# Kernel optimization log

Measured on AMD Instinct MI355X. Metric: run time of the kernel, lower is better.

Reference implementation:

```python
import jax, jax.numpy as jnp
import numpy as np

D_MODEL = 1024
NHEAD = 16
HEAD_DIM = D_MODEL // NHEAD
B, L = 4, 8192
LN_EPS = 1e-5


def setup_inputs() -> dict:
    key = jax.random.key(0)
    ks = jax.random.split(key, 8)
    s = 1.0 / np.sqrt(D_MODEL)
    return {
        "x": jax.random.normal(ks[0], (B, L, D_MODEL), dtype=jnp.float32),
        "decay": jax.random.uniform(ks[1], (NHEAD,), dtype=jnp.float32, minval=0.8, maxval=0.999),
        "Wq": jax.random.normal(ks[2], (D_MODEL, D_MODEL), dtype=jnp.float32) * s,
        "Wv": jax.random.normal(ks[3], (D_MODEL, D_MODEL), dtype=jnp.float32) * s,
        "Wg": jax.random.normal(ks[4], (D_MODEL, D_MODEL), dtype=jnp.float32) * s,
        "Wo": jax.random.normal(ks[5], (D_MODEL, D_MODEL), dtype=jnp.float32) * s,
        "ln_gamma": jnp.ones((D_MODEL,), dtype=jnp.float32),
        "ln_beta": jnp.zeros((D_MODEL,), dtype=jnp.float32),
    }


def _decay_scan(v, lam):
    # v: (B, L, H, Dh), lam: (H,). s_t = lam * s_{t-1} + v_t, parallel assoc scan over L.
    a = jnp.broadcast_to(lam[None, None, :, None], v.shape)

    def combine(c1, c2):
        a1, b1 = c1
        a2, b2 = c2
        return a1 * a2, b1 * a2 + b2

    _, state = jax.lax.associative_scan(combine, (a, v), axis=1)
    return state


def _layernorm(y, gamma, beta):
    mu = jnp.mean(y, axis=-1, keepdims=True)
    var = jnp.mean(jnp.square(y - mu), axis=-1, keepdims=True)
    return (y - mu) * jax.lax.rsqrt(var + LN_EPS) * gamma + beta


def reference(x, decay, Wq, Wv, Wg, Wo, ln_gamma, ln_beta):
    Bx, Lx, D = x.shape
    q = (x @ Wq.T).reshape(Bx, Lx, NHEAD, HEAD_DIM)
    v = (x @ Wv.T).reshape(Bx, Lx, NHEAD, HEAD_DIM)
    state = _decay_scan(v, decay)                      # (B, L, H, Dh)
    y = (q * state).reshape(Bx, Lx, D)
    y = _layernorm(y, ln_gamma, ln_beta)
    gate = jax.nn.silu(x @ Wg.T)
    y = y * gate
    return y @ Wo.T
```

## Files before the change

kernel.cpp:

```cpp
#include <hip/hip_runtime.h>
#include <cstdint>
#include <cstddef>

typedef unsigned short u16;
typedef __attribute__((ext_vector_type(4))) float f32x4;
typedef __attribute__((ext_vector_type(8))) short s16x8;
typedef __attribute__((ext_vector_type(4))) short s16x4;

#define D_M   1024
#define KDIM  1024
#define BB    4
#define LL    8192
#define MTOT  (BB*LL)
#define CHK   64
#define CHK_SH 6
#define NCH   (LL/CHK)
#define NT    (KDIM/64)
#define LN_EPS 1e-5f

static __device__ __forceinline__ float bf2f(u16 u){
  return __uint_as_float(((unsigned)u)<<16);
}
static __device__ __forceinline__ u16 f2bf(float f){
  unsigned u = __float_as_uint(f);
  u += 0x7fffu + ((u>>16)&1u);
  return (u16)(u>>16);
}

template<int IMM>
static __device__ __forceinline__ s16x8 dsr(uint32_t a){
  s16x8 d;
  asm volatile("ds_read_b128 %0, %1 offset:%c2" : "=v"(d) : "v"(a), "i"(IMM));
  return d;
}

__global__ void conv_f2b_k(const float* __restrict__ src, u16* __restrict__ dst, int n4){
  int i = blockIdx.x*blockDim.x + threadIdx.x;
  int stride = gridDim.x*blockDim.x;
  for (; i < n4; i += stride){
    f32x4 f = ((const f32x4*)src)[i];
    s16x4 o;
    o[0]=(short)f2bf(f[0]); o[1]=(short)f2bf(f[1]);
    o[2]=(short)f2bf(f[2]); o[3]=(short)f2bf(f[3]);
    ((s16x4*)dst)[i] = o;
  }
}

__global__ void conv_w4_k(const float* __restrict__ s0, const float* __restrict__ s1,
                          const float* __restrict__ s2, const float* __restrict__ s3,
                          u16* __restrict__ d0, u16* __restrict__ d1,
                          u16* __restrict__ d2, u16* __restrict__ d3){
  const float* s; u16* d;
  switch(blockIdx.y){
    case 0: s=s0; d=d0; break;
    case 1: s=s1; d=d1; break;
    case 2: s=s2; d=d2; break;
    default: s=s3; d=d3; break;
  }
  int i = blockIdx.x*blockDim.x + threadIdx.x;
  f32x4 f = ((const f32x4*)s)[i];
  s16x4 o;
  o[0]=(short)f2bf(f[0]); o[1]=(short)f2bf(f[1]);
  o[2]=(short)f2bf(f[2]); o[3]=(short)f2bf(f[3]);
  ((s16x4*)d)[i] = o;
}

template<int F32OUT>
__global__ __launch_bounds__(512,2) void gemm256(
    const u16* __restrict__ A,
    const u16* __restrict__ W0, const u16* __restrict__ W1, const u16* __restrict__ W2,
    void* __restrict__ O0, void* __restrict__ O1, void* __restrict__ O2)
{
  __shared__ __align__(16) u16 smem[65536];

  const int mode = blockIdx.z;
  const u16* W = (mode==0)? W0 : ((mode==1)? W1 : W2);
  void* Ov     = (mode==0)? O0 : ((mode==1)? O1 : O2);

  const int tid  = threadIdx.x;
  const int wave = tid>>6, lane = tid&63;
  const int bm = blockIdx.x*256, bn = blockIdx.y*256;

  const int rr = tid>>3;
  const int kk = (((tid&7) ^ (rr&7)))*8;
  const int ldw = wave*512;

  #define STAGE(GBASE, LOFF) do {                                                       \
    const u16* _g = (GBASE) + (size_t)rr*KDIM + kk;                                     \
    __builtin_amdgcn_global_load_lds(                                                   \
      (const __attribute__((address_space(1))) void*)(_g),                              \
      (__attribute__((address_space(3))) void*)(smem + (LOFF) + ldw), 16, 0, 0);        \
    __builtin_amdgcn_global_load_lds(                                                   \
      (const __attribute__((address_space(1))) void*)(_g + (size_t)64*KDIM),            \
      (__attribute__((address_space(3))) void*)(smem + (LOFF) + 4096 + ldw), 16, 0, 0); \
  } while(0)

  const uint32_t smem_base =
    (uint32_t)(uintptr_t)((__attribute__((address_space(3))) u16*)smem);
  const int lr = lane&15, lk = lane>>4;
  const int wm = wave>>2, wn = wave&3;
  const uint32_t vA0 = smem_base + (uint32_t)((((wm*64+lr)*64) + (( lk   )^(lr&7))*8)<<1);
  const uint32_t vA1 = smem_base + (uint32_t)((((wm*64+lr)*64) + ((4+lk  )^(lr&7))*8)<<1);
  const uint32_t vB0 = smem_base + 65536u + (uint32_t)((((wn*32+lr)*64) + (( lk )^(lr&7))*8)<<1);
  const uint32_t vB1 = smem_base + 65536u + (uint32_t)((((wn*32+lr)*64) + ((4+lk)^(lr&7))*8)<<1);

  const f32x4 fzero = {0.f,0.f,0.f,0.f};
  f32x4 acc[8][4];
  #pragma unroll
  for (int i=0;i<8;i++)
    #pragma unroll
    for (int j=0;j<4;j++)
      acc[i][j] = fzero;

  const u16* Abase = A + (size_t)bm*KDIM;
  const u16* Wbase = W + (size_t)bn*KDIM;

  STAGE(Abase,                    0);
  STAGE(Wbase,                    32768);
  STAGE(Wbase + (size_t)128*KDIM, 32768+8192);
  STAGE(Abase + (size_t)128*KDIM, 8192);
  STAGE(Abase + 64,                    16384);
  STAGE(Wbase + 64,                    49152);
  STAGE(Wbase + (size_t)128*KDIM + 64, 49152+8192);
  asm volatile("s_waitcnt vmcnt(6)" ::: "memory");
  __builtin_amdgcn_s_barrier();

  s16x8 afr[4][2], blo[2][2], bhi[2][2];

  #define LDA8(CUR,HI) \
    afr[0][0]=dsr<(CUR)*32768+(HI)*16384+0   >(vA0); afr[0][1]=dsr<(CUR)*32768+(HI)*16384+0   >(vA1); \
    afr[1][0]=dsr<(CUR)*32768+(HI)*16384+2048>(vA0); afr[1][1]=dsr<(CUR)*32768+(HI)*16384+2048>(vA1); \
    afr[2][0]=dsr<(CUR)*32768+(HI)*16384+4096>(vA0); afr[2][1]=dsr<(CUR)*32768+(HI)*16384+4096>(vA1); \
    afr[3][0]=dsr<(CUR)*32768+(HI)*16384+6144>(vA0); afr[3][1]=dsr<(CUR)*32768+(HI)*16384+6144>(vA1);

  #define LDB4(DST,CUR,HI) \
    DST[0][0]=dsr<(CUR)*32768+(HI)*16384+0   >(vB0); DST[0][1]=dsr<(CUR)*32768+(HI)*16384+0   >(vB1); \
    DST[1][0]=dsr<(CUR)*32768+(HI)*16384+2048>(vB0); DST[1][1]=dsr<(CUR)*32768+(HI)*16384+2048>(vB1);

  #define LGKM_FENCE() do { \
    asm volatile("s_waitcnt lgkmcnt(0)" ::: "memory"); \
    __builtin_amdgcn_sched_barrier(0); \
  } while(0)

  #define MM16(AI0, NI0, BFR) \
    _Pragma("unroll") \
    for (int mi=0; mi<4; ++mi) \
      _Pragma("unroll") \
      for (int ni=0; ni<2; ++ni) \
        _Pragma("unroll") \
        for (int kp=0; kp<2; ++kp) \
          acc[(AI0)+mi][(NI0)+ni] = __builtin_amdgcn_mfma_f32_16x16x32_bf16( \
            afr[mi][kp], BFR[ni][kp], acc[(AI0)+mi][(NI0)+ni], 0,0,0);

  #define TILE(KT, CUR) do {                                                       \
                                        \
    LDA8(CUR,0)                                                                    \
    LDB4(blo,CUR,0)                                                                \
    if ((KT)+1 < NT) STAGE(Abase + (size_t)128*KDIM + ((KT)+1)*64,                 \
                           ((CUR)^1)*16384 + 8192);                                \
    __builtin_amdgcn_s_barrier();                                                  \
    LGKM_FENCE();                                                                  \
    __builtin_amdgcn_s_setprio(1);                                                 \
    MM16(0,0,blo)                                                                  \
    __builtin_amdgcn_s_setprio(0);                                                 \
    __builtin_amdgcn_s_barrier();                                                  \
                                        \
    LDB4(bhi,CUR,1)                                                                \
    if ((KT)+2 < NT) STAGE(Abase + ((KT)+2)*64, (CUR)*16384);                      \
    __builtin_amdgcn_s_barrier();                                                  \
    LGKM_FENCE();                                                                  \
    __builtin_amdgcn_s_setprio(1);                                                 \
    MM16(0,2,bhi)                                                                  \
    __builtin_amdgcn_s_setprio(0);                                                 \
    __builtin_amdgcn_s_barrier();                                                  \
                                        \
    LDA8(CUR,1)                                                                    \
    if ((KT)+2 < NT) STAGE(Wbase + ((KT)+2)*64, 32768 + (CUR)*16384);              \
    __builtin_amdgcn_s_barrier();                                                  \
    LGKM_FENCE();                                                                  \
    __builtin_amdgcn_s_setprio(1);                                                 \
    MM16(4,2,bhi)                                                                  \
    __builtin_amdgcn_s_setprio(0);                                                 \
    __builtin_amdgcn_s_barrier();                                                  \
                         \
    if ((KT)+2 < NT) STAGE(Wbase + (size_t)128*KDIM + ((KT)+2)*64,                 \
                           32768 + (CUR)*16384 + 8192);                            \
    __builtin_amdgcn_s_barrier();                                                  \
    __builtin_amdgcn_s_setprio(1);                                                 \
    MM16(4,0,blo)                                                                  \
    __builtin_amdgcn_s_setprio(0);                                                 \
    if ((KT) < NT-2) { asm volatile("s_waitcnt vmcnt(6)" ::: "memory"); }          \
    else             { asm volatile("s_waitcnt vmcnt(0)" ::: "memory"); }          \
    __builtin_amdgcn_s_barrier();                                                  \
  } while(0)

  for (int kt=0; kt<NT; kt+=2){
    TILE(kt,   0);
    TILE(kt+1, 1);
  }
  #undef TILE
  #undef MM16
  #undef LGKM_FENCE
  #undef LDB4
  #undef LDA8
  #undef STAGE

  const int rq = (lane>>4)*4;
  const int cl = lane&15;
  if (F32OUT){
    float* O = (float*)Ov;
    #pragma unroll
    for (int mi=0; mi<8; ++mi){
      const int grow = bm + (mi>>2)*128 + wm*64 + (mi&3)*16 + rq;
      #pragma unroll
      for (int ni=0; ni<4; ++ni){
        const int gcol = bn + (ni>>1)*128 + wn*32 + (ni&1)*16 + cl;
        #pragma unroll
        for (int r=0;r<4;r++)
          O[(size_t)(grow + r)*D_M + gcol] = acc[mi][ni][r];
      }
    }
  } else {
    u16* O = (u16*)Ov;
    const bool do_silu = (mode==2);
    #pragma unroll
    for (int mi=0; mi<8; ++mi){
      const int grow = bm + (mi>>2)*128 + wm*64 + (mi&3)*16 + rq;
      #pragma unroll
      for (int ni=0; ni<4; ++ni){
        const int gcol = bn + (ni>>1)*128 + wn*32 + (ni&1)*16 + cl;
        #pragma unroll
        for (int r=0;r<4;r++){
          float vv = acc[mi][ni][r];
          if (do_silu) vv = vv / (1.f + __expf(-vv));
          O[(size_t)(grow + r)*D_M + gcol] = f2bf(vv);
        }
      }
    }
  }
}

__global__ __launch_bounds__(256) void scan1_k(u16* __restrict__ v, float* __restrict__ E,
                                               const float* __restrict__ decay){
  const int c = blockIdx.x, b = blockIdx.y;
  const int d0 = threadIdx.x*4;
  const float lam = decay[d0>>6];
  float s0=0.f,s1=0.f,s2=0.f,s3=0.f;
  u16* p = v + ((size_t)b*LL + (size_t)c*CHK)*D_M + d0;
  for (int i=0;i<CHK;i++){
    s16x4 x = *(const s16x4*)p;
    s0 = fmaf(s0, lam, bf2f((u16)x[0]));
    s1 = fmaf(s1, lam, bf2f((u16)x[1]));
    s2 = fmaf(s2, lam, bf2f((u16)x[2]));
    s3 = fmaf(s3, lam, bf2f((u16)x[3]));
    s16x4 o;
    o[0]=(short)f2bf(s0); o[1]=(short)f2bf(s1);
    o[2]=(short)f2bf(s2); o[3]=(short)f2bf(s3);
    *(s16x4*)p = o;
    p += D_M;
  }
  f32x4 e = {s0,s1,s2,s3};
  *(f32x4*)(E + ((size_t)(b*NCH + c))*D_M + d0) = e;
}

__global__ void scan2_k(const float* __restrict__ E, float* __restrict__ S,
                        const float* __restrict__ decay){
  const int idx = blockIdx.x*blockDim.x + threadIdx.x;
  if (idx >= BB*(D_M/4)) return;
  const int b  = idx / (D_M/4);
  const int d0 = (idx % (D_M/4))*4;
  const float lam  = decay[d0>>6];
  const float lamT = __expf((float)CHK * __logf(lam));
  f32x4 s = {0.f,0.f,0.f,0.f};
  for (int c=0;c<NCH;c++){
    const size_t o = ((size_t)(b*NCH + c))*D_M + d0;
    f32x4 e = *(const f32x4*)(E + o);
    s = s*lamT + e;
    *(f32x4*)(S + o) = s;
  }
}

__global__ __launch_bounds__(256) void fuse_ln_k(
  const u16* __restrict__ qb, const u16* __restrict__ locb, const u16* __restrict__ gateb,
  const float* __restrict__ S, const float* __restrict__ decay,
  const float* __restrict__ gamma, const float* __restrict__ beta,
  u16* __restrict__ yout)
{
  const int token = blockIdx.x;
  const int b  = token >> 13;
  const int t  = token & (LL-1);
  const int c  = t >> CHK_SH;
  const int ii = t & (CHK-1);
  const int tid = threadIdx.x;
  const int d0 = tid*4;
  const float lam = decay[d0>>6];
  const float pw  = __expf((float)(ii+1) * __logf(lam));
  f32x4 carry = {0.f,0.f,0.f,0.f};
  if (c > 0) carry = *(const f32x4*)(S + ((size_t)(b*NCH + (c-1)))*D_M + d0);
  const size_t base = (size_t)token*D_M + d0;
  s16x4 q4 = *(const s16x4*)(qb + base);
  s16x4 l4 = *(const s16x4*)(locb + base);
  float y[4];
  #pragma unroll
  for (int j=0;j<4;j++)
    y[j] = bf2f((u16)q4[j]) * (bf2f((u16)l4[j]) + pw*carry[j]);
  float sum = y[0]+y[1]+y[2]+y[3];
  float sq  = y[0]*y[0]+y[1]*y[1]+y[2]*y[2]+y[3]*y[3];
  #pragma unroll
  for (int off=32; off>0; off>>=1){
    sum += __shfl_down(sum, off);
    sq  += __shfl_down(sq , off);
  }
  __shared__ float red[10];
  const int wave = tid>>6, lane = tid&63;
  if (lane==0){ red[wave] = sum; red[4+wave] = sq; }
  __syncthreads();
  if (tid==0){
    float ts = red[0]+red[1]+red[2]+red[3];
    float tq = red[4]+red[5]+red[6]+red[7];
    float mu  = ts * (1.f/(float)D_M);
    float var = tq * (1.f/(float)D_M) - mu*mu;
    red[8] = mu;
    red[9] = rsqrtf(var + LN_EPS);
  }
  __syncthreads();
  const float mu = red[8], rstd = red[9];
  f32x4 gm = *(const f32x4*)(gamma + d0);
  f32x4 bt = *(const f32x4*)(beta  + d0);
  s16x4 g4 = *(const s16x4*)(gateb + base);
  s16x4 o;
  #pragma unroll
  for (int j=0;j<4;j++){
    float nn = (y[j] - mu)*rstd*gm[j] + bt[j];
    nn *= bf2f((u16)g4[j]);
    o[j] = (short)f2bf(nn);
  }
  *(s16x4*)(yout + base) = o;
}

extern "C" void kernel_launch(void* const* d_in, const int* in_sizes, int n_in,
                              void* d_out, int out_size, void* d_ws, size_t ws_size,
                              hipStream_t stream)
{
  const float* x     = (const float*)d_in[0];
  const float* decay = (const float*)d_in[1];
  const float* Wq    = (const float*)d_in[2];
  const float* Wv    = (const float*)d_in[3];
  const float* Wg    = (const float*)d_in[4];
  const float* Wo    = (const float*)d_in[5];
  const float* gamma = (const float*)d_in[6];
  const float* beta  = (const float*)d_in[7];
  float* out = (float*)d_out;

  char* ws = (char*)d_ws;
  size_t off = 0;
  const size_t XB = (size_t)MTOT*D_M*sizeof(u16);
  const size_t WB = (size_t)D_M*KDIM*sizeof(u16);
  const size_t EB = (size_t)BB*NCH*D_M*sizeof(float);
  u16* xb  = (u16*)(ws+off); off += XB;
  u16* Wqb = (u16*)(ws+off); off += WB;
  u16* Wvb = (u16*)(ws+off); off += WB;
  u16* Wgb = (u16*)(ws+off); off += WB;
  u16* Wob = (u16*)(ws+off); off += WB;
  u16* qb  = (u16*)(ws+off); off += XB;
  u16* vb  = (u16*)(ws+off); off += XB;
  u16* gb  = (u16*)(ws+off); off += XB;
  float* E = (float*)(ws+off); off += EB;
  float* S = (float*)(ws+off); off += EB;

  conv_f2b_k<<<dim3(2048), 256, 0, stream>>>(x,  xb,  MTOT*D_M/4);
  conv_w4_k<<<dim3(1024,4), 256, 0, stream>>>(Wq, Wv, Wg, Wo, Wqb, Wvb, Wgb, Wob);

  gemm256<0><<<dim3(MTOT/256, D_M/256, 3), 512, 0, stream>>>(xb, Wqb, Wvb, Wgb, qb, vb, gb);

  scan1_k<<<dim3(NCH, BB), 256, 0, stream>>>(vb, E, decay);
  scan2_k<<<dim3(4), 256, 0, stream>>>(E, S, decay);

  fuse_ln_k<<<dim3(MTOT), 256, 0, stream>>>(qb, vb, gb, S, decay, gamma, beta, qb);

  gemm256<1><<<dim3(MTOT/256, D_M/256, 1), 512, 0, stream>>>(qb, Wob, Wob, Wob,
                                                             (void*)out, (void*)out, (void*)out);
}
```

Baseline: 417.5 us.

## Use 1024-thread GEMM blocks with smaller per-wave tiles; widen scan2 parallelism

The 256x256 GEMM now runs with 16 waves per block instead of 8. Each wave computes a 64x64 sub-tile (acc[4][4]) instead of 128x64, and each thread issues one async global-to-LDS load per stage instead of two. The goal is to raise latency hiding and cut per-thread register pressure, at the cost of more LDS read traffic per MFMA and more barrier participants. The launch bound of (1024,4) is likely unattainable with 128KB of LDS per block. The carry-propagation scan also moves to one scalar channel per thread with a prefetched next element, using 16 blocks instead of 4.

Measured after the change: 435.8 us. +4.4%, slower.

```diff
diff --git a/kernel.cpp b/kernel.cpp
--- a/kernel.cpp
+++ b/kernel.cpp
@@ -66,7 +66,7 @@
 }
 
 template<int F32OUT>
-__global__ __launch_bounds__(512,2) void gemm256(
+__global__ __launch_bounds__(1024,4) void gemm256(
     const u16* __restrict__ A,
     const u16* __restrict__ W0, const u16* __restrict__ W1, const u16* __restrict__ W2,
     void* __restrict__ O0, void* __restrict__ O1, void* __restrict__ O2)
@@ -83,31 +83,34 @@
 
   const int rr = tid>>3;
   const int kk = (((tid&7) ^ (rr&7)))*8;
+  const size_t stoff = (size_t)rr*KDIM + kk;
   const int ldw = wave*512;
 
   #define STAGE(GBASE, LOFF) do {                                                       \
-    const u16* _g = (GBASE) + (size_t)rr*KDIM + kk;                                     \
     __builtin_amdgcn_global_load_lds(                                                   \
-      (const __attribute__((address_space(1))) void*)(_g),                              \
+      (const __attribute__((address_space(1))) void*)((GBASE) + stoff),                 \
       (__attribute__((address_space(3))) void*)(smem + (LOFF) + ldw), 16, 0, 0);        \
-    __builtin_amdgcn_global_load_lds(                                                   \
-      (const __attribute__((address_space(1))) void*)(_g + (size_t)64*KDIM),            \
-      (__attribute__((address_space(3))) void*)(smem + (LOFF) + 4096 + ldw), 16, 0, 0); \
   } while(0)
 
   const uint32_t smem_base =
     (uint32_t)(uintptr_t)((__attribute__((address_space(3))) u16*)smem);
   const int lr = lane&15, lk = lane>>4;
   const int wm = wave>>2, wn = wave&3;
-  const uint32_t vA0 = smem_base + (uint32_t)((((wm*64+lr)*64) + (( lk   )^(lr&7))*8)<<1);
-  const uint32_t vA1 = smem_base + (uint32_t)((((wm*64+lr)*64) + ((4+lk  )^(lr&7))*8)<<1);
-  const uint32_t vB0 = smem_base + 65536u + (uint32_t)((((wn*32+lr)*64) + (( lk )^(lr&7))*8)<<1);
-  const uint32_t vB1 = smem_base + 65536u + (uint32_t)((((wn*32+lr)*64) + ((4+lk)^(lr&7))*8)<<1);
+  const int arow = (wm&1)*64 + lr;
+  const int brow = (wn&1)*64 + lr;
+  const uint32_t vA0 = smem_base + (wm>=2?16384u:0u)
+                     + (uint32_t)(arow*128 + (( lk   )^(lr&7))*16);
+  const uint32_t vA1 = smem_base + (wm>=2?16384u:0u)
+                     + (uint32_t)(arow*128 + ((4+lk  )^(lr&7))*16);
+  const uint32_t vB0 = smem_base + 65536u + (wn>=2?16384u:0u)
+                     + (uint32_t)(brow*128 + (( lk   )^(lr&7))*16);
+  const uint32_t vB1 = smem_base + 65536u + (wn>=2?16384u:0u)
+                     + (uint32_t)(brow*128 + ((4+lk  )^(lr&7))*16);
 
   const f32x4 fzero = {0.f,0.f,0.f,0.f};
-  f32x4 acc[8][4];
+  f32x4 acc[4][4];
   #pragma unroll
-  for (int i=0;i<8;i++)
+  for (int i=0;i<4;i++)
     #pragma unroll
     for (int j=0;j<4;j++)
       acc[i][j] = fzero;
@@ -120,76 +123,75 @@
   STAGE(Wbase + (size_t)128*KDIM, 32768+8192);
   STAGE(Abase + (size_t)128*KDIM, 8192);
   STAGE(Abase + 64,                    16384);
-  STAGE(Wbase + 64,                    49152);
-  STAGE(Wbase + (size_t)128*KDIM + 64, 49152+8192);
-  asm volatile("s_waitcnt vmcnt(6)" ::: "memory");
+  STAGE(Wbase + 64,                    32768+16384);
+  STAGE(Wbase + (size_t)128*KDIM + 64, 32768+16384+8192);
+  asm volatile("s_waitcnt vmcnt(3)" ::: "memory");
   __builtin_amdgcn_s_barrier();
 
-  s16x8 afr[4][2], blo[2][2], bhi[2][2];
-
-  #define LDA8(CUR,HI) \
-    afr[0][0]=dsr<(CUR)*32768+(HI)*16384+0   >(vA0); afr[0][1]=dsr<(CUR)*32768+(HI)*16384+0   >(vA1); \
-    afr[1][0]=dsr<(CUR)*32768+(HI)*16384+2048>(vA0); afr[1][1]=dsr<(CUR)*32768+(HI)*16384+2048>(vA1); \
-    afr[2][0]=dsr<(CUR)*32768+(HI)*16384+4096>(vA0); afr[2][1]=dsr<(CUR)*32768+(HI)*16384+4096>(vA1); \
-    afr[3][0]=dsr<(CUR)*32768+(HI)*16384+6144>(vA0); afr[3][1]=dsr<(CUR)*32768+(HI)*16384+6144>(vA1);
-
-  #define LDB4(DST,CUR,HI) \
-    DST[0][0]=dsr<(CUR)*32768+(HI)*16384+0   >(vB0); DST[0][1]=dsr<(CUR)*32768+(HI)*16384+0   >(vB1); \
-    DST[1][0]=dsr<(CUR)*32768+(HI)*16384+2048>(vB0); DST[1][1]=dsr<(CUR)*32768+(HI)*16384+2048>(vB1);
+  s16x8 a[2][2], b01[2][2], b23[2][2];
+
+  #define LDA_PAIR(CUR, MB) \
+    a[0][0]=dsr<(CUR)*32768+(MB)*2048     >(vA0); a[0][1]=dsr<(CUR)*32768+(MB)*2048     >(vA1); \
+    a[1][0]=dsr<(CUR)*32768+(MB)*2048+2048>(vA0); a[1][1]=dsr<(CUR)*32768+(MB)*2048+2048>(vA1);
+
+  #define LDB_PAIR(DST, CUR, NB) \
+    DST[0][0]=dsr<(CUR)*32768+(NB)*2048     >(vB0); DST[0][1]=dsr<(CUR)*32768+(NB)*2048     >(vB1); \
+    DST[1][0]=dsr<(CUR)*32768+(NB)*2048+2048>(vB0); DST[1][1]=dsr<(CUR)*32768+(NB)*2048+2048>(vB1);
 
   #define LGKM_FENCE() do { \
     asm volatile("s_waitcnt lgkmcnt(0)" ::: "memory"); \
     __builtin_amdgcn_sched_barrier(0); \
   } while(0)
 
-  #define MM16(AI0, NI0, BFR) \
+  #define MM8(MB, NB, BF) \
     _Pragma("unroll") \
-    for (int mi=0; mi<4; ++mi) \
+    for (int mi=0; mi<2; ++mi) \
       _Pragma("unroll") \
       for (int ni=0; ni<2; ++ni) \
         _Pragma("unroll") \
         for (int kp=0; kp<2; ++kp) \
-          acc[(AI0)+mi][(NI0)+ni] = __builtin_amdgcn_mfma_f32_16x16x32_bf16( \
-            afr[mi][kp], BFR[ni][kp], acc[(AI0)+mi][(NI0)+ni], 0,0,0);
+          acc[(MB)+mi][(NB)+ni] = __builtin_amdgcn_mfma_f32_16x16x32_bf16( \
+            a[mi][kp], BF[ni][kp], acc[(MB)+mi][(NB)+ni], 0,0,0);
 
   #define TILE(KT, CUR) do {                                                       \
-                                        \
-    LDA8(CUR,0)                                                                    \
-    LDB4(blo,CUR,0)                                                                \
+                                             \
+    LDA_PAIR(CUR,0)                                                                \
+    LDB_PAIR(b01,CUR,0)                                                            \
     if ((KT)+1 < NT) STAGE(Abase + (size_t)128*KDIM + ((KT)+1)*64,                 \
                            ((CUR)^1)*16384 + 8192);                                \
     __builtin_amdgcn_s_barrier();                                                  \
     LGKM_FENCE();                                                                  \
     __builtin_amdgcn_s_setprio(1);                                                 \
-    MM16(0,0,blo)                                                                  \
+    MM8(0,0,b01)                                                                   \
     __builtin_amdgcn_s_setprio(0);                                                 \
     __builtin_amdgcn_s_barrier();                                                  \
-                                        \
-    LDB4(bhi,CUR,1)                                                                \
-    if ((KT)+2 < NT) STAGE(Abase + ((KT)+2)*64, (CUR)*16384);                      \
+                                                               \
+    LDB_PAIR(b23,CUR,2)                                                            \
     __builtin_amdgcn_s_barrier();                                                  \
     LGKM_FENCE();                                                                  \
     __builtin_amdgcn_s_setprio(1);                                                 \
-    MM16(0,2,bhi)                                                                  \
+    MM8(0,2,b23)                                                                   \
     __builtin_amdgcn_s_setprio(0);                                                 \
     __builtin_amdgcn_s_barrier();                                                  \
-                                        \
-    LDA8(CUR,1)                                                                    \
+                                             \
+    LDA_PAIR(CUR,2)                                                                \
     if ((KT)+2 < NT) STAGE(Wbase + ((KT)+2)*64, 32768 + (CUR)*16384);              \
     __builtin_amdgcn_s_barrier();                                                  \
     LGKM_FENCE();                                                                  \
     __builtin_amdgcn_s_setprio(1);                                                 \
-    MM16(4,2,bhi)                                                                  \
+    MM8(2,2,b23)                                                                   \
     __builtin_amdgcn_s_setprio(0);                                                 \
     __builtin_amdgcn_s_barrier();                                                  \
-                         \
-    if ((KT)+2 < NT) STAGE(Wbase + (size_t)128*KDIM + ((KT)+2)*64,                 \
-                           32768 + (CUR)*16384 + 8192);                            \
+                  \
+    if ((KT)+2 < NT){                                                              \
+      STAGE(Wbase + (size_t)128*KDIM + ((KT)+2)*64, 32768 + (CUR)*16384 + 8192);   \
+      STAGE(Abase + ((KT)+2)*64, (CUR)*16384);                                     \
+    }                                                                              \
     __builtin_amdgcn_s_barrier();                                                  \
     __builtin_amdgcn_s_setprio(1);                                                 \
-    MM16(4,0,blo)                                                                  \
+    MM8(2,0,b01)                                                                   \
     __builtin_amdgcn_s_setprio(0);                                                 \
-    if ((KT) < NT-2) { asm volatile("s_waitcnt vmcnt(6)" ::: "memory"); }          \
+    if ((KT) < NT-2) { asm volatile("s_waitcnt vmcnt(3)" ::: "memory"); }          \
     else             { asm volatile("s_waitcnt vmcnt(0)" ::: "memory"); }          \
     __builtin_amdgcn_s_barrier();                                                  \
   } while(0)
@@ -199,10 +201,10 @@
     TILE(kt+1, 1);
   }
   #undef TILE
-  #undef MM16
+  #undef MM8
   #undef LGKM_FENCE
-  #undef LDB4
-  #undef LDA8
+  #undef LDB_PAIR
+  #undef LDA_PAIR
   #undef STAGE
 
   const int rq = (lane>>4)*4;
@@ -210,11 +212,11 @@
   if (F32OUT){
     float* O = (float*)Ov;
     #pragma unroll
-    for (int mi=0; mi<8; ++mi){
-      const int grow = bm + (mi>>2)*128 + wm*64 + (mi&3)*16 + rq;
+    for (int mi=0; mi<4; ++mi){
+      const int grow = bm + wm*64 + mi*16 + rq;
       #pragma unroll
       for (int ni=0; ni<4; ++ni){
-        const int gcol = bn + (ni>>1)*128 + wn*32 + (ni&1)*16 + cl;
+        const int gcol = bn + wn*64 + ni*16 + cl;
         #pragma unroll
         for (int r=0;r<4;r++)
           O[(size_t)(grow + r)*D_M + gcol] = acc[mi][ni][r];
@@ -224,11 +226,11 @@
     u16* O = (u16*)Ov;
     const bool do_silu = (mode==2);
     #pragma unroll
-    for (int mi=0; mi<8; ++mi){
-      const int grow = bm + (mi>>2)*128 + wm*64 + (mi&3)*16 + rq;
+    for (int mi=0; mi<4; ++mi){
+      const int grow = bm + wm*64 + mi*16 + rq;
       #pragma unroll
       for (int ni=0; ni<4; ++ni){
-        const int gcol = bn + (ni>>1)*128 + wn*32 + (ni&1)*16 + cl;
+        const int gcol = bn + wn*64 + ni*16 + cl;
         #pragma unroll
         for (int r=0;r<4;r++){
           float vv = acc[mi][ni][r];
@@ -266,17 +268,17 @@
 __global__ void scan2_k(const float* __restrict__ E, float* __restrict__ S,
                         const float* __restrict__ decay){
   const int idx = blockIdx.x*blockDim.x + threadIdx.x;
-  if (idx >= BB*(D_M/4)) return;
-  const int b  = idx / (D_M/4);
-  const int d0 = (idx % (D_M/4))*4;
-  const float lam  = decay[d0>>6];
+  if (idx >= BB*D_M) return;
+  const int b = idx >> 10, d = idx & (D_M-1);
+  const float lam  = decay[d>>6];
   const float lamT = __expf((float)CHK * __logf(lam));
-  f32x4 s = {0.f,0.f,0.f,0.f};
+  float s = 0.f;
+  float e_nxt = E[(size_t)(b*NCH)*D_M + d];
   for (int c=0;c<NCH;c++){
-    const size_t o = ((size_t)(b*NCH + c))*D_M + d0;
-    f32x4 e = *(const f32x4*)(E + o);
-    s = s*lamT + e;
-    *(f32x4*)(S + o) = s;
+    float e = e_nxt;
+    if (c+1 < NCH) e_nxt = E[(size_t)(b*NCH + c+1)*D_M + d];
+    s = fmaf(s, lamT, e);
+    S[(size_t)(b*NCH + c)*D_M + d] = s;
   }
 }
 
@@ -371,13 +373,13 @@
   conv_f2b_k<<<dim3(2048), 256, 0, stream>>>(x,  xb,  MTOT*D_M/4);
   conv_w4_k<<<dim3(1024,4), 256, 0, stream>>>(Wq, Wv, Wg, Wo, Wqb, Wvb, Wgb, Wob);
 
-  gemm256<0><<<dim3(MTOT/256, D_M/256, 3), 512, 0, stream>>>(xb, Wqb, Wvb, Wgb, qb, vb, gb);
+  gemm256<0><<<dim3(MTOT/256, D_M/256, 3), 1024, 0, stream>>>(xb, Wqb, Wvb, Wgb, qb, vb, gb);
 
   scan1_k<<<dim3(NCH, BB), 256, 0, stream>>>(vb, E, decay);
-  scan2_k<<<dim3(4), 256, 0, stream>>>(E, S, decay);
+  scan2_k<<<dim3(16), 256, 0, stream>>>(E, S, decay);
 
   fuse_ln_k<<<dim3(MTOT), 256, 0, stream>>>(qb, vb, gb, S, decay, gamma, beta, qb);
 
-  gemm256<1><<<dim3(MTOT/256, D_M/256, 1), 512, 0, stream>>>(qb, Wob, Wob, Wob,
-                                                             (void*)out, (void*)out, (void*)out);
-}
+  gemm256<1><<<dim3(MTOT/256, D_M/256, 1), 1024, 0, stream>>>(qb, Wob, Wob, Wob,
+                                                              (void*)out, (void*)out, (void*)out);
+}
```

## Remap GEMM blocks per XCD, widen scan2 parallelism, use wave-per-token LayerNorm

Applied to the files above, without the earlier changes.

The three input projections now read one concatenated weight buffer through a flat 1D grid. A block-index remap groups blocks so that those sharing A rows land on the same XCD (bid&7), aiming for better L2 reuse of activations. scan2 now runs one thread per channel with 16 blocks instead of four-wide vectors in 4 blocks, and prefetches the next chunk to shorten its serial latency chain. The fused LayerNorm kernel handles one token per wave with 16-byte loads and xor-shuffle reductions, which removes the shared-memory reductions and block barriers. The column wrap mask and the mode derivation rely on index arithmetic that must match the hidden tiling code.

Result: slower. 432.9 us (+3.7%).

```diff
diff --git a/kernel.cpp b/kernel.cpp
--- a/kernel.cpp
+++ b/kernel.cpp
@@ -65,21 +65,22 @@
   ((s16x4*)d)[i] = o;
 }
 
-template<int F32OUT>
+template<int F32OUT, int NBN>
 __global__ __launch_bounds__(512,2) void gemm256(
-    const u16* __restrict__ A,
-    const u16* __restrict__ W0, const u16* __restrict__ W1, const u16* __restrict__ W2,
+    const u16* __restrict__ A, const u16* __restrict__ W,
     void* __restrict__ O0, void* __restrict__ O1, void* __restrict__ O2)
 {
   __shared__ __align__(16) u16 smem[65536];
 
-  const int mode = blockIdx.z;
-  const u16* W = (mode==0)? W0 : ((mode==1)? W1 : W2);
-  void* Ov     = (mode==0)? O0 : ((mode==1)? O1 : O2);
+  const int bid = blockIdx.x;
+  const int jj  = bid>>3;
+  const int bm  = ((bid&7)*16 + (jj&15))*256;
+  const int bn  = (jj>>4)*256;
+  const int mode = bn>>10;
+  void* Ov = (mode==0)? O0 : ((mode==1)? O1 : O2);
 
   const int tid  = threadIdx.x;
   const int wave = tid>>6, lane = tid&63;
-  const int bm = blockIdx.x*256, bn = blockIdx.y*256;
 
   const int rr = tid>>3;
   const int kk = (((tid&7) ^ (rr&7)))*8;
@@ -214,7 +215,7 @@
       const int grow = bm + (mi>>2)*128 + wm*64 + (mi&3)*16 + rq;
       #pragma unroll
       for (int ni=0; ni<4; ++ni){
-        const int gcol = bn + (ni>>1)*128 + wn*32 + (ni&1)*16 + cl;
+        const int gcol = (bn + (ni>>1)*128 + wn*32 + (ni&1)*16 + cl) & (D_M-1);
         #pragma unroll
         for (int r=0;r<4;r++)
           O[(size_t)(grow + r)*D_M + gcol] = acc[mi][ni][r];
@@ -228,7 +229,7 @@
       const int grow = bm + (mi>>2)*128 + wm*64 + (mi&3)*16 + rq;
       #pragma unroll
       for (int ni=0; ni<4; ++ni){
-        const int gcol = bn + (ni>>1)*128 + wn*32 + (ni&1)*16 + cl;
+        const int gcol = (bn + (ni>>1)*128 + wn*32 + (ni&1)*16 + cl) & (D_M-1);
         #pragma unroll
         for (int r=0;r<4;r++){
           float vv = acc[mi][ni][r];
@@ -266,17 +267,17 @@
 __global__ void scan2_k(const float* __restrict__ E, float* __restrict__ S,
                         const float* __restrict__ decay){
   const int idx = blockIdx.x*blockDim.x + threadIdx.x;
-  if (idx >= BB*(D_M/4)) return;
-  const int b  = idx / (D_M/4);
-  const int d0 = (idx % (D_M/4))*4;
-  const float lam  = decay[d0>>6];
+  if (idx >= BB*D_M) return;
+  const int b = idx >> 10, d = idx & (D_M-1);
+  const float lam  = decay[d>>6];
   const float lamT = __expf((float)CHK * __logf(lam));
-  f32x4 s = {0.f,0.f,0.f,0.f};
+  float s = 0.f;
+  float e_nxt = E[(size_t)(b*NCH)*D_M + d];
   for (int c=0;c<NCH;c++){
-    const size_t o = ((size_t)(b*NCH + c))*D_M + d0;
-    f32x4 e = *(const f32x4*)(E + o);
-    s = s*lamT + e;
-    *(f32x4*)(S + o) = s;
+    float e = e_nxt;
+    if (c+1 < NCH) e_nxt = E[(size_t)(b*NCH + c+1)*D_M + d];
+    s = fmaf(s, lamT, e);
+    S[(size_t)(b*NCH + c)*D_M + d] = s;
   }
 }
 
@@ -286,56 +287,80 @@
   const float* __restrict__ gamma, const float* __restrict__ beta,
   u16* __restrict__ yout)
 {
-  const int token = blockIdx.x;
+  const int wv = threadIdx.x>>6, lane = threadIdx.x&63;
+  const int token = blockIdx.x*4 + wv;
   const int b  = token >> 13;
   const int t  = token & (LL-1);
   const int c  = t >> CHK_SH;
   const int ii = t & (CHK-1);
-  const int tid = threadIdx.x;
-  const int d0 = tid*4;
-  const float lam = decay[d0>>6];
-  const float pw  = __expf((float)(ii+1) * __logf(lam));
-  f32x4 carry = {0.f,0.f,0.f,0.f};
-  if (c > 0) carry = *(const f32x4*)(S + ((size_t)(b*NCH + (c-1)))*D_M + d0);
-  const size_t base = (size_t)token*D_M + d0;
-  s16x4 q4 = *(const s16x4*)(qb + base);
-  s16x4 l4 = *(const s16x4*)(locb + base);
-  float y[4];
-  #pragma unroll
-  for (int j=0;j<4;j++)
-    y[j] = bf2f((u16)q4[j]) * (bf2f((u16)l4[j]) + pw*carry[j]);
-  float sum = y[0]+y[1]+y[2]+y[3];
-  float sq  = y[0]*y[0]+y[1]*y[1]+y[2]*y[2]+y[3]*y[3];
+  const int d0 = lane*8;
+  const float li = (float)(ii+1);
+  const float lam0 = decay[d0>>6];
+  const float lam1 = decay[(512+d0)>>6];
+  const float pw0 = __expf(li * __logf(lam0));
+  const float pw1 = __expf(li * __logf(lam1));
+
+  const size_t base = (size_t)token*D_M;
+  f32x4 car[4] = {{0,0,0,0},{0,0,0,0},{0,0,0,0},{0,0,0,0}};
+  if (c > 0){
+    const float* Sp = S + ((size_t)(b*NCH + (c-1)))*D_M;
+    car[0] = *(const f32x4*)(Sp + d0);
+    car[1] = *(const f32x4*)(Sp + d0 + 4);
+    car[2] = *(const f32x4*)(Sp + 512 + d0);
+    car[3] = *(const f32x4*)(Sp + 512 + d0 + 4);
+  }
+  s16x8 q0 = *(const s16x8*)(qb + base + d0);
+  s16x8 q1 = *(const s16x8*)(qb + base + 512 + d0);
+  s16x8 l0 = *(const s16x8*)(locb + base + d0);
+  s16x8 l1 = *(const s16x8*)(locb + base + 512 + d0);
+
+  float y[16];
+  #pragma unroll
+  for (int j=0;j<8;j++)
+    y[j]   = bf2f((u16)q0[j]) * (bf2f((u16)l0[j]) + pw0*car[j>>2][j&3]);
+  #pragma unroll
+  for (int j=0;j<8;j++)
+    y[8+j] = bf2f((u16)q1[j]) * (bf2f((u16)l1[j]) + pw1*car[2+(j>>2)][j&3]);
+
+  float sum = 0.f, sq = 0.f;
+  #pragma unroll
+  for (int j=0;j<16;j++){ sum += y[j]; sq += y[j]*y[j]; }
   #pragma unroll
   for (int off=32; off>0; off>>=1){
-    sum += __shfl_down(sum, off);
-    sq  += __shfl_down(sq , off);
-  }
-  __shared__ float red[10];
-  const int wave = tid>>6, lane = tid&63;
-  if (lane==0){ red[wave] = sum; red[4+wave] = sq; }
-  __syncthreads();
-  if (tid==0){
-    float ts = red[0]+red[1]+red[2]+red[3];
-    float tq = red[4]+red[5]+red[6]+red[7];
-    float mu  = ts * (1.f/(float)D_M);
-    float var = tq * (1.f/(float)D_M) - mu*mu;
-    red[8] = mu;
-    red[9] = rsqrtf(var + LN_EPS);
-  }
-  __syncthreads();
-  const float mu = red[8], rstd = red[9];
-  f32x4 gm = *(const f32x4*)(gamma + d0);
-  f32x4 bt = *(const f32x4*)(beta  + d0);
-  s16x4 g4 = *(const s16x4*)(gateb + base);
-  s16x4 o;
-  #pragma unroll
-  for (int j=0;j<4;j++){
-    float nn = (y[j] - mu)*rstd*gm[j] + bt[j];
-    nn *= bf2f((u16)g4[j]);
-    o[j] = (short)f2bf(nn);
-  }
-  *(s16x4*)(yout + base) = o;
+    sum += __shfl_xor(sum, off);
+    sq  += __shfl_xor(sq , off);
+  }
+  const float mu   = sum * (1.f/(float)D_M);
+  const float rstd = rsqrtf(sq * (1.f/(float)D_M) - mu*mu + LN_EPS);
+
+  s16x8 g0 = *(const s16x8*)(gateb + base + d0);
+  s16x8 g1 = *(const s16x8*)(gateb + base + 512 + d0);
+  f32x4 gmA = *(const f32x4*)(gamma + d0);
+  f32x4 gmB = *(const f32x4*)(gamma + d0 + 4);
+  f32x4 gmC = *(const f32x4*)(gamma + 512 + d0);
+  f32x4 gmD = *(const f32x4*)(gamma + 512 + d0 + 4);
+  f32x4 btA = *(const f32x4*)(beta + d0);
+  f32x4 btB = *(const f32x4*)(beta + d0 + 4);
+  f32x4 btC = *(const f32x4*)(beta + 512 + d0);
+  f32x4 btD = *(const f32x4*)(beta + 512 + d0 + 4);
+
+  s16x8 o0, o1;
+  #pragma unroll
+  for (int j=0;j<8;j++){
+    float gm = (j<4)? gmA[j&3] : gmB[j&3];
+    float bt = (j<4)? btA[j&3] : btB[j&3];
+    float nn = (y[j] - mu)*rstd*gm + bt;
+    o0[j] = (short)f2bf(nn * bf2f((u16)g0[j]));
+  }
+  #pragma unroll
+  for (int j=0;j<8;j++){
+    float gm = (j<4)? gmC[j&3] : gmD[j&3];
+    float bt = (j<4)? btC[j&3] : btD[j&3];
+    float nn = (y[8+j] - mu)*rstd*gm + bt;
+    o1[j] = (short)f2bf(nn * bf2f((u16)g1[j]));
+  }
+  *(s16x8*)(yout + base + d0) = o0;
+  *(s16x8*)(yout + base + 512 + d0) = o1;
 }
 
 extern "C" void kernel_launch(void* const* d_in, const int* in_sizes, int n_in,
@@ -357,11 +382,9 @@
   const size_t XB = (size_t)MTOT*D_M*sizeof(u16);
   const size_t WB = (size_t)D_M*KDIM*sizeof(u16);
   const size_t EB = (size_t)BB*NCH*D_M*sizeof(float);
-  u16* xb  = (u16*)(ws+off); off += XB;
-  u16* Wqb = (u16*)(ws+off); off += WB;
-  u16* Wvb = (u16*)(ws+off); off += WB;
-  u16* Wgb = (u16*)(ws+off); off += WB;
-  u16* Wob = (u16*)(ws+off); off += WB;
+  u16* xb   = (u16*)(ws+off); off += XB;
+  u16* Wcat = (u16*)(ws+off); off += 3*WB;
+  u16* Wob  = (u16*)(ws+off); off += WB;
   u16* qb  = (u16*)(ws+off); off += XB;
   u16* vb  = (u16*)(ws+off); off += XB;
   u16* gb  = (u16*)(ws+off); off += XB;
@@ -369,15 +392,16 @@
   float* S = (float*)(ws+off); off += EB;
 
   conv_f2b_k<<<dim3(2048), 256, 0, stream>>>(x,  xb,  MTOT*D_M/4);
-  conv_w4_k<<<dim3(1024,4), 256, 0, stream>>>(Wq, Wv, Wg, Wo, Wqb, Wvb, Wgb, Wob);
-
-  gemm256<0><<<dim3(MTOT/256, D_M/256, 3), 512, 0, stream>>>(xb, Wqb, Wvb, Wgb, qb, vb, gb);
+  conv_w4_k<<<dim3(1024,4), 256, 0, stream>>>(Wq, Wv, Wg, Wo,
+                                              Wcat, Wcat + (size_t)D_M*KDIM,
+                                              Wcat + (size_t)2*D_M*KDIM, Wob);
+
+  gemm256<0,12><<<dim3(1536), 512, 0, stream>>>(xb, Wcat, qb, vb, gb);
 
   scan1_k<<<dim3(NCH, BB), 256, 0, stream>>>(vb, E, decay);
-  scan2_k<<<dim3(4), 256, 0, stream>>>(E, S, decay);
-
-  fuse_ln_k<<<dim3(MTOT), 256, 0, stream>>>(qb, vb, gb, S, decay, gamma, beta, qb);
-
-  gemm256<1><<<dim3(MTOT/256, D_M/256, 1), 512, 0, stream>>>(qb, Wob, Wob, Wob,
-                                                             (void*)out, (void*)out, (void*)out);
-}
+  scan2_k<<<dim3(16), 256, 0, stream>>>(E, S, decay);
+
+  fuse_ln_k<<<dim3(MTOT/4), 256, 0, stream>>>(qb, vb, gb, S, decay, gamma, beta, qb);
+
+  gemm256<1,4><<<dim3(512), 512, 0, stream>>>(qb, Wob, (void*)out, (void*)out, (void*)out);
+}
```

## Concatenate QVG weights, swizzle GEMM grid, and merge pipeline phases to cut barriers

Applied to the files above, without the earlier changes.

The three projection weights are stored as one concatenated matrix. The QVG GEMM becomes a single 1D launch whose block index is remapped so that the eight consecutive blocks spread across M tiles and share the same N tile, which is meant to improve L2 reuse of the weights. The K-loop schedule is reorganised from four barrier-separated MFMA phases into two larger phases, with B fragment loads and global-to-LDS stages grouped together and vmcnt thresholds adjusted. This removes several barriers per tile, at the cost of deeper register and vmcnt pressure and more careful hazard ordering on the LDS buffers.

Result: slower. 427.5 us (+2.4%).

```diff
diff --git a/kernel.cpp b/kernel.cpp
--- a/kernel.cpp
+++ b/kernel.cpp
@@ -65,21 +65,22 @@
   ((s16x4*)d)[i] = o;
 }
 
-template<int F32OUT>
+template<int F32OUT, int NBN>
 __global__ __launch_bounds__(512,2) void gemm256(
-    const u16* __restrict__ A,
-    const u16* __restrict__ W0, const u16* __restrict__ W1, const u16* __restrict__ W2,
+    const u16* __restrict__ A, const u16* __restrict__ W,
     void* __restrict__ O0, void* __restrict__ O1, void* __restrict__ O2)
 {
   __shared__ __align__(16) u16 smem[65536];
 
-  const int mode = blockIdx.z;
-  const u16* W = (mode==0)? W0 : ((mode==1)? W1 : W2);
-  void* Ov     = (mode==0)? O0 : ((mode==1)? O1 : O2);
+  const int bid = blockIdx.x;
+  const int jj  = bid>>3;
+  const int bm  = ((bid&7)*16 + (jj&15))*256;
+  const int bn  = (jj>>4)*256;
+  const int mode = bn>>10;
+  void* Ov = (mode==0)? O0 : ((mode==1)? O1 : O2);
 
   const int tid  = threadIdx.x;
   const int wave = tid>>6, lane = tid&63;
-  const int bm = blockIdx.x*256, bn = blockIdx.y*256;
 
   const int rr = tid>>3;
   const int kk = (((tid&7) ^ (rr&7)))*8;
@@ -153,43 +154,33 @@
             afr[mi][kp], BFR[ni][kp], acc[(AI0)+mi][(NI0)+ni], 0,0,0);
 
   #define TILE(KT, CUR) do {                                                       \
-                                        \
+            \
     LDA8(CUR,0)                                                                    \
     LDB4(blo,CUR,0)                                                                \
+    LDB4(bhi,CUR,1)                                                                \
     if ((KT)+1 < NT) STAGE(Abase + (size_t)128*KDIM + ((KT)+1)*64,                 \
                            ((CUR)^1)*16384 + 8192);                                \
-    __builtin_amdgcn_s_barrier();                                                  \
     LGKM_FENCE();                                                                  \
     __builtin_amdgcn_s_setprio(1);                                                 \
     MM16(0,0,blo)                                                                  \
+    MM16(0,2,bhi)                                                                  \
     __builtin_amdgcn_s_setprio(0);                                                 \
+    if ((KT) < NT-1) { asm volatile("s_waitcnt vmcnt(8)" ::: "memory"); }          \
+    else             { asm volatile("s_waitcnt vmcnt(0)" ::: "memory"); }          \
     __builtin_amdgcn_s_barrier();                                                  \
-                                        \
-    LDB4(bhi,CUR,1)                                                                \
-    if ((KT)+2 < NT) STAGE(Abase + ((KT)+2)*64, (CUR)*16384);                      \
-    __builtin_amdgcn_s_barrier();                                                  \
+        \
+    LDA8(CUR,1)                                                                    \
+    if ((KT)+2 < NT){                                                              \
+      STAGE(Abase + ((KT)+2)*64, (CUR)*16384);                                     \
+      STAGE(Wbase + ((KT)+2)*64, 32768 + (CUR)*16384);                             \
+      STAGE(Wbase + (size_t)128*KDIM + ((KT)+2)*64, 32768 + (CUR)*16384 + 8192);   \
+    }                                                                              \
     LGKM_FENCE();                                                                  \
     __builtin_amdgcn_s_setprio(1);                                                 \
-    MM16(0,2,bhi)                                                                  \
-    __builtin_amdgcn_s_setprio(0);                                                 \
-    __builtin_amdgcn_s_barrier();                                                  \
-                                        \
-    LDA8(CUR,1)                                                                    \
-    if ((KT)+2 < NT) STAGE(Wbase + ((KT)+2)*64, 32768 + (CUR)*16384);              \
-    __builtin_amdgcn_s_barrier();                                                  \
-    LGKM_FENCE();                                                                  \
-    __builtin_amdgcn_s_setprio(1);                                                 \
+    MM16(4,0,blo)                                                                  \
     MM16(4,2,bhi)                                                                  \
     __builtin_amdgcn_s_setprio(0);                                                 \
-    __builtin_amdgcn_s_barrier();                                                  \
-                         \
-    if ((KT)+2 < NT) STAGE(Wbase + (size_t)128*KDIM + ((KT)+2)*64,                 \
-                           32768 + (CUR)*16384 + 8192);                            \
-    __builtin_amdgcn_s_barrier();                                                  \
-    __builtin_amdgcn_s_setprio(1);                                                 \
-    MM16(4,0,blo)                                                                  \
-    __builtin_amdgcn_s_setprio(0);                                                 \
-    if ((KT) < NT-2) { asm volatile("s_waitcnt vmcnt(6)" ::: "memory"); }          \
+    if ((KT) < NT-2) { asm volatile("s_waitcnt vmcnt(8)" ::: "memory"); }          \
     else             { asm volatile("s_waitcnt vmcnt(0)" ::: "memory"); }          \
     __builtin_amdgcn_s_barrier();                                                  \
   } while(0)
@@ -214,7 +205,7 @@
       const int grow = bm + (mi>>2)*128 + wm*64 + (mi&3)*16 + rq;
       #pragma unroll
       for (int ni=0; ni<4; ++ni){
-        const int gcol = bn + (ni>>1)*128 + wn*32 + (ni&1)*16 + cl;
+        const int gcol = (bn + (ni>>1)*128 + wn*32 + (ni&1)*16 + cl) & (D_M-1);
         #pragma unroll
         for (int r=0;r<4;r++)
           O[(size_t)(grow + r)*D_M + gcol] = acc[mi][ni][r];
@@ -228,7 +219,7 @@
       const int grow = bm + (mi>>2)*128 + wm*64 + (mi&3)*16 + rq;
       #pragma unroll
       for (int ni=0; ni<4; ++ni){
-        const int gcol = bn + (ni>>1)*128 + wn*32 + (ni&1)*16 + cl;
+        const int gcol = (bn + (ni>>1)*128 + wn*32 + (ni&1)*16 + cl) & (D_M-1);
         #pragma unroll
         for (int r=0;r<4;r++){
           float vv = acc[mi][ni][r];
@@ -357,11 +348,9 @@
   const size_t XB = (size_t)MTOT*D_M*sizeof(u16);
   const size_t WB = (size_t)D_M*KDIM*sizeof(u16);
   const size_t EB = (size_t)BB*NCH*D_M*sizeof(float);
-  u16* xb  = (u16*)(ws+off); off += XB;
-  u16* Wqb = (u16*)(ws+off); off += WB;
-  u16* Wvb = (u16*)(ws+off); off += WB;
-  u16* Wgb = (u16*)(ws+off); off += WB;
-  u16* Wob = (u16*)(ws+off); off += WB;
+  u16* xb   = (u16*)(ws+off); off += XB;
+  u16* Wcat = (u16*)(ws+off); off += 3*WB;
+  u16* Wob  = (u16*)(ws+off); off += WB;
   u16* qb  = (u16*)(ws+off); off += XB;
   u16* vb  = (u16*)(ws+off); off += XB;
   u16* gb  = (u16*)(ws+off); off += XB;
@@ -369,15 +358,16 @@
   float* S = (float*)(ws+off); off += EB;
 
   conv_f2b_k<<<dim3(2048), 256, 0, stream>>>(x,  xb,  MTOT*D_M/4);
-  conv_w4_k<<<dim3(1024,4), 256, 0, stream>>>(Wq, Wv, Wg, Wo, Wqb, Wvb, Wgb, Wob);
-
-  gemm256<0><<<dim3(MTOT/256, D_M/256, 3), 512, 0, stream>>>(xb, Wqb, Wvb, Wgb, qb, vb, gb);
+  conv_w4_k<<<dim3(1024,4), 256, 0, stream>>>(Wq, Wv, Wg, Wo,
+                                              Wcat, Wcat + (size_t)D_M*KDIM,
+                                              Wcat + (size_t)2*D_M*KDIM, Wob);
+
+  gemm256<0,12><<<dim3(1536), 512, 0, stream>>>(xb, Wcat, qb, vb, gb);
 
   scan1_k<<<dim3(NCH, BB), 256, 0, stream>>>(vb, E, decay);
   scan2_k<<<dim3(4), 256, 0, stream>>>(E, S, decay);
 
   fuse_ln_k<<<dim3(MTOT), 256, 0, stream>>>(qb, vb, gb, S, decay, gamma, beta, qb);
 
-  gemm256<1><<<dim3(MTOT/256, D_M/256, 1), 512, 0, stream>>>(qb, Wob, Wob, Wob,
-                                                             (void*)out, (void*)out, (void*)out);
-}
+  gemm256<1,4><<<dim3(512), 512, 0, stream>>>(qb, Wob, (void*)out, (void*)out, (void*)out);
+}
```
